# Kernel optimization log

Measured on AMD Instinct MI355X. Metric: run time of the kernel, lower is better.

Reference implementation:

```python
import jax, jax.numpy as jnp
import numpy as np

NUM_EMBEDDINGS = 1024  # num_gestures
EMBEDDING_DIM = 512    # win_size * num_pellets = 32 * 16


def setup_inputs() -> dict:
    key = jax.random.key(0)
    k1, k2 = jax.random.split(key)
    inputs = jax.random.normal(k1, (64, 512, EMBEDDING_DIM), dtype=jnp.float32)
    weight = jax.random.normal(k2, (NUM_EMBEDDINGS, EMBEDDING_DIM), dtype=jnp.float32)
    return {"inputs": inputs, "weight": weight}


def reference(inputs, weight):
    input_shape = inputs.shape
    flat = inputs.reshape(-1, EMBEDDING_DIM)  # [N, D]
    distances = (
        jnp.sum(flat * flat, axis=1, keepdims=True)
        + jnp.sum(weight * weight, axis=1)
        - 2.0 * (flat @ weight.T)
    )
    encoding_indices = jnp.argmin(distances, axis=1)  # [N]
    # one-hot @ weight is just a gather of codebook rows
    quantized = weight[encoding_indices].reshape(input_shape)
    loss_vq = jnp.mean((quantized - inputs) ** 2)
    return loss_vq
```

## Files before the change

### kernel.cpp

```cpp
#include <hip/hip_runtime.h>
#include <hip/hip_bf16.h>
#include <stdint.h>

typedef __attribute__((ext_vector_type(4))) int i32x4;

#define N_ROWS  32768
#define N_CODES 1024
#define DIM     512

typedef const __attribute__((address_space(1))) uint32_t guint;
typedef __attribute__((address_space(3))) uint32_t luint;
static __device__ __forceinline__ void gl_lds16(const char* g, char* l) {
    __builtin_amdgcn_global_load_lds((guint*)g, (luint*)l, 16, 0, 0);
}

static __device__ __forceinline__ int q8(float v) {
    int q = __float2int_rn(v * 32.0f);
    return max(-127, min(127, q));
}

__global__ void __launch_bounds__(256)
convertXW(const float* __restrict__ X, const float* __restrict__ W,
          char* __restrict__ Xq, char* __restrict__ Wq,
          float* __restrict__ xnorm, float* __restrict__ wnorm) {
    const int lane = threadIdx.x & 63;
    const int sub  = threadIdx.x >> 6;
    const float* src; char* dst; float* nrm; int row;
    if (blockIdx.x < 8192) {
        row = blockIdx.x * 4 + sub;
        src = X; dst = Xq; nrm = xnorm;
    } else {
        row = (blockIdx.x - 8192) * 4 + sub;
        src = W; dst = Wq; nrm = wnorm;
    }
    const float4* p = (const float4*)(src + (size_t)row * DIM + lane * 8);
    float4 a = p[0], b = p[1];
    uint32_t lo = (uint32_t)(q8(a.x) & 0xFF)
                | ((uint32_t)(q8(a.y) & 0xFF) << 8)
                | ((uint32_t)(q8(a.z) & 0xFF) << 16)
                | ((uint32_t)(q8(a.w) & 0xFF) << 24);
    uint32_t hi = (uint32_t)(q8(b.x) & 0xFF)
                | ((uint32_t)(q8(b.y) & 0xFF) << 8)
                | ((uint32_t)(q8(b.z) & 0xFF) << 16)
                | ((uint32_t)(q8(b.w) & 0xFF) << 24);
    *(uint2*)(dst + (size_t)row * DIM + lane * 8) = make_uint2(lo, hi);
    float s = a.x*a.x + a.y*a.y + a.z*a.z + a.w*a.w
            + b.x*b.x + b.y*b.y + b.z*b.z + b.w*b.w;
    #pragma unroll
    for (int d = 1; d < 64; d <<= 1) s += __shfl_xor(s, d);
    if (lane == 0) nrm[row] = s;
}

__global__ void __launch_bounds__(256, 2)
gemm_argmin(const char* __restrict__ Xq, const char* __restrict__ Wq,
            const float* __restrict__ wnorm, const float* __restrict__ xnorm,
            float* __restrict__ partial) {
    __shared__ __align__(16) char As[8 * 4096];
    __shared__ __align__(16) char Bs[4 * 3 * 4096];

    const int tid  = threadIdx.x;
    const int lane = tid & 63;
    const int wave = tid >> 6;
    const int lr = lane & 15, kg = lane >> 4;

    const int bid = blockIdx.x;
    const int rowBase = ((bid & 7) * 64 + (bid >> 3)) * 64;
    const int colW = wave * 256;

    const int ssw = ((lane & 3) ^ ((lane >> 3) & 3)) * 16;
    const char* aS = Xq + (size_t)(rowBase + wave * 16 + (lane >> 2)) * DIM + ssw;
    const char* bS = Wq + (size_t)(colW + (lane >> 2)) * DIM + ssw;
    char* bD = Bs + wave * 12288 + lane * 16;

#define STAGE_B(s) do {                                                       \
    const int ctp_ = (s) >> 3, kt_ = (s) & 7, buf_ = (s) % 3;                 \
    _Pragma("unroll")                                                         \
    for (int j = 0; j < 4; ++j)                                               \
        gl_lds16(bS + (size_t)(ctp_ * 64 + j * 16) * DIM + kt_ * 64,          \
                 bD + buf_ * 4096 + j * 1024);                                \
  } while (0)

    #pragma unroll
    for (int kt = 0; kt < 8; ++kt)
        gl_lds16(aS + kt * 64, As + kt * 4096 + wave * 1024 + lane * 16);
    STAGE_B(0);
    STAGE_B(1);
    asm volatile("s_waitcnt vmcnt(4)" ::: "memory");
    __syncthreads();

    i32x4 acc[4][4];
    #pragma unroll
    for (int m = 0; m < 4; ++m)
        #pragma unroll
        for (int n = 0; n < 4; ++n) acc[m][n] = (i32x4)0;
    uint32_t runKey[4][4];
    #pragma unroll
    for (int m = 0; m < 4; ++m)
        #pragma unroll
        for (int r = 0; r < 4; ++r) runKey[m][r] = 0xFFFFFFFFu;

    const int fq = (kg ^ ((lr >> 1) & 3)) * 16;
    const char* bR = Bs + wave * 12288;

    for (int ctp = 0; ctp < 4; ++ctp) {
        #pragma unroll
        for (int kt = 0; kt < 8; ++kt) {
            const int s = ctp * 8 + kt;
            const int buf = s % 3;
            i32x4 aF[4], bF[4];
            #pragma unroll
            for (int m = 0; m < 4; ++m)
                aF[m] = *(const i32x4*)&As[kt * 4096 + (m * 16 + lr) * 64 + fq];
            #pragma unroll
            for (int n = 0; n < 4; ++n)
                bF[n] = *(const i32x4*)&bR[buf * 4096 + (n * 16 + lr) * 64 + fq];
            if (s + 2 < 32) STAGE_B(s + 2);
            #pragma unroll
            for (int m = 0; m < 4; ++m)
                #pragma unroll
                for (int n = 0; n < 4; ++n)
                    acc[m][n] = __builtin_amdgcn_mfma_i32_16x16x64_i8(
                        aF[m], bF[n], acc[m][n], 0, 0, 0);
            if (s + 2 < 32)   asm volatile("s_waitcnt vmcnt(4)" ::: "memory");
            else if (s == 30) asm volatile("s_waitcnt vmcnt(0)" ::: "memory");
        }
        #pragma unroll
        for (int n = 0; n < 4; ++n) {
            const int wcol = colW + ctp * 64 + n * 16 + lr;
            const float wn = wnorm[wcol];
            #pragma unroll
            for (int m = 0; m < 4; ++m)
                #pragma unroll
                for (int r = 0; r < 4; ++r) {
                    float sc = wn - (float)acc[m][n][r] * 0.001953125f;
                    uint32_t u = __float_as_uint(sc);
                    u = (u & 0x80000000u) ? ~u : (u | 0x80000000u);
                    runKey[m][r] = min(runKey[m][r],
                                       (u & ~1023u) | (uint32_t)wcol);
                }
        }
        #pragma unroll
        for (int m = 0; m < 4; ++m)
            #pragma unroll
            for (int n = 0; n < 4; ++n) acc[m][n] = (i32x4)0;
    }
#undef STAGE_B

    uint32_t* kbuf = (uint32_t*)(Bs + wave * 12288);
    #pragma unroll
    for (int m = 0; m < 4; ++m)
        #pragma unroll
        for (int r = 0; r < 4; ++r) {
            uint32_t k = runKey[m][r];
            #pragma unroll
            for (int d = 1; d < 16; d <<= 1)
                k = min(k, (uint32_t)__shfl_xor((int)k, d));
            if (lr == 0) kbuf[m * 16 + kg * 4 + r] = k;
        }
    __syncthreads();

    if (wave == 0) {
        const uint32_t* k0 = (const uint32_t*)(Bs);
        uint32_t k = min(min(k0[lane], k0[3072 + lane]),
                         min(k0[6144 + lane], k0[9216 + lane]));
        uint32_t sb = k & ~1023u;
        float sc = (sb & 0x80000000u) ? __uint_as_float(sb ^ 0x80000000u)
                                      : __uint_as_float(~sb);
        float v = xnorm[rowBase + lane] + sc;
        #pragma unroll
        for (int d = 1; d < 64; d <<= 1) v += __shfl_xor(v, d);
        if (lane == 0) partial[bid] = v;
    }
}

__global__ void __launch_bounds__(256)
finalize(const float* __restrict__ partial, float* __restrict__ out) {
    __shared__ double sm[256];
    sm[threadIdx.x] = (double)partial[threadIdx.x]
                    + (double)partial[threadIdx.x + 256];
    __syncthreads();
    for (int st = 128; st > 0; st >>= 1) {
        if (threadIdx.x < st) sm[threadIdx.x] += sm[threadIdx.x + st];
        __syncthreads();
    }
    if (threadIdx.x == 0)
        out[0] = (float)(sm[0] / (double)((size_t)N_ROWS * DIM));
}

extern "C" void kernel_launch(void* const* d_in, const int* in_sizes, int n_in,
                              void* d_out, int out_size, void* d_ws, size_t ws_size,
                              hipStream_t stream) {
    const float* X = (const float*)d_in[0];
    const float* W = (const float*)d_in[1];
    char* ws = (char*)d_ws;
    char*   Xq      = ws;
    char*   Wq      = ws + 16777216;
    float*  wnorm   = (float*)(ws + 17301504);
    float*  xnorm   = (float*)(ws + 17305600);
    float*  partial = (float*)(ws + 17436672);
    float*  out     = (float*)d_out;

    convertXW<<<8192 + N_CODES / 4, 256, 0, stream>>>(X, W, Xq, Wq, xnorm, wnorm);
    gemm_argmin<<<512, 256, 0, stream>>>(Xq, Wq, wnorm, xnorm, partial);
    finalize<<<1, 256, 0, stream>>>(partial, out);
}
```

Measured before the change: 48.56 us.

## Fuse X quantization and norm computation into the GEMM-argmin kernel

The standalone conversion pass over X is removed. Each GEMM block now loads its 64 fp32 rows directly, computes row norms, quantizes them to int8 and writes them into swizzled LDS. This avoids writing and re-reading the 16MB int8 copy of X plus the xnorm array, and the convert kernel now handles only W. In exchange, the X load in the GEMM prologue is synchronous fp32 register traffic that no longer overlaps with the async B staging as the old global_load_lds path did.

```diff
diff --git a/kernel.cpp b/kernel.cpp
--- a/kernel.cpp
+++ b/kernel.cpp
@@ -18,43 +18,30 @@
     int q = __float2int_rn(v * 32.0f);
     return max(-127, min(127, q));
 }
+static __device__ __forceinline__ uint32_t pack4(float a, float b, float c, float d) {
+    return (uint32_t)(q8(a) & 0xFF) | ((uint32_t)(q8(b) & 0xFF) << 8)
+         | ((uint32_t)(q8(c) & 0xFF) << 16) | ((uint32_t)(q8(d) & 0xFF) << 24);
+}
 
 __global__ void __launch_bounds__(256)
-convertXW(const float* __restrict__ X, const float* __restrict__ W,
-          char* __restrict__ Xq, char* __restrict__ Wq,
-          float* __restrict__ xnorm, float* __restrict__ wnorm) {
+convertW(const float* __restrict__ W, char* __restrict__ Wq,
+         float* __restrict__ wnorm) {
     const int lane = threadIdx.x & 63;
-    const int sub  = threadIdx.x >> 6;
-    const float* src; char* dst; float* nrm; int row;
-    if (blockIdx.x < 8192) {
-        row = blockIdx.x * 4 + sub;
-        src = X; dst = Xq; nrm = xnorm;
-    } else {
-        row = (blockIdx.x - 8192) * 4 + sub;
-        src = W; dst = Wq; nrm = wnorm;
-    }
-    const float4* p = (const float4*)(src + (size_t)row * DIM + lane * 8);
+    const int code = blockIdx.x * 4 + (threadIdx.x >> 6);
+    const float4* p = (const float4*)(W + (size_t)code * DIM + lane * 8);
     float4 a = p[0], b = p[1];
-    uint32_t lo = (uint32_t)(q8(a.x) & 0xFF)
-                | ((uint32_t)(q8(a.y) & 0xFF) << 8)
-                | ((uint32_t)(q8(a.z) & 0xFF) << 16)
-                | ((uint32_t)(q8(a.w) & 0xFF) << 24);
-    uint32_t hi = (uint32_t)(q8(b.x) & 0xFF)
-                | ((uint32_t)(q8(b.y) & 0xFF) << 8)
-                | ((uint32_t)(q8(b.z) & 0xFF) << 16)
-                | ((uint32_t)(q8(b.w) & 0xFF) << 24);
-    *(uint2*)(dst + (size_t)row * DIM + lane * 8) = make_uint2(lo, hi);
+    *(uint2*)(Wq + (size_t)code * DIM + lane * 8) =
+        make_uint2(pack4(a.x, a.y, a.z, a.w), pack4(b.x, b.y, b.z, b.w));
     float s = a.x*a.x + a.y*a.y + a.z*a.z + a.w*a.w
             + b.x*b.x + b.y*b.y + b.z*b.z + b.w*b.w;
     #pragma unroll
     for (int d = 1; d < 64; d <<= 1) s += __shfl_xor(s, d);
-    if (lane == 0) nrm[row] = s;
+    if (lane == 0) wnorm[code] = s;
 }
 
 __global__ void __launch_bounds__(256, 2)
-gemm_argmin(const char* __restrict__ Xq, const char* __restrict__ Wq,
-            const float* __restrict__ wnorm, const float* __restrict__ xnorm,
-            float* __restrict__ partial) {
+gemm_argmin(const float* __restrict__ X, const char* __restrict__ Wq,
+            const float* __restrict__ wnorm, float* __restrict__ partial) {
     __shared__ __align__(16) char As[8 * 4096];
     __shared__ __align__(16) char Bs[4 * 3 * 4096];
 
@@ -68,7 +55,6 @@
     const int colW = wave * 256;
 
     const int ssw = ((lane & 3) ^ ((lane >> 3) & 3)) * 16;
-    const char* aS = Xq + (size_t)(rowBase + wave * 16 + (lane >> 2)) * DIM + ssw;
     const char* bS = Wq + (size_t)(colW + (lane >> 2)) * DIM + ssw;
     char* bD = Bs + wave * 12288 + lane * 16;
 
@@ -80,12 +66,34 @@
                  bD + buf_ * 4096 + j * 1024);                                \
   } while (0)
 
-    #pragma unroll
-    for (int kt = 0; kt < 8; ++kt)
-        gl_lds16(aS + kt * 64, As + kt * 4096 + wave * 1024 + lane * 16);
     STAGE_B(0);
     STAGE_B(1);
-    asm volatile("s_waitcnt vmcnt(4)" ::: "memory");
+
+    const int r = tid >> 2, q4 = tid & 3;
+    const int rsw = (r >> 1) & 3;
+    float nrm = 0.f;
+    {
+        const float* xP = X + (size_t)(rowBase + r) * DIM + q4 * 128;
+        #pragma unroll
+        for (int c = 0; c < 8; ++c) {
+            float4 f0 = *(const float4*)(xP + c * 16);
+            float4 f1 = *(const float4*)(xP + c * 16 + 4);
+            float4 f2 = *(const float4*)(xP + c * 16 + 8);
+            float4 f3 = *(const float4*)(xP + c * 16 + 12);
+            nrm += f0.x*f0.x + f0.y*f0.y + f0.z*f0.z + f0.w*f0.w
+                 + f1.x*f1.x + f1.y*f1.y + f1.z*f1.z + f1.w*f1.w
+                 + f2.x*f2.x + f2.y*f2.y + f2.z*f2.z + f2.w*f2.w
+                 + f3.x*f3.x + f3.y*f3.y + f3.z*f3.z + f3.w*f3.w;
+            i32x4 v = { (int)pack4(f0.x, f0.y, f0.z, f0.w),
+                        (int)pack4(f1.x, f1.y, f1.z, f1.w),
+                        (int)pack4(f2.x, f2.y, f2.z, f2.w),
+                        (int)pack4(f3.x, f3.y, f3.z, f3.w) };
+            const int kt = 2 * q4 + (c >> 2), sl = c & 3;
+            *(i32x4*)&As[kt * 4096 + r * 64 + (sl ^ rsw) * 16] = v;
+        }
+        nrm += __shfl_xor(nrm, 1);
+        nrm += __shfl_xor(nrm, 2);
+    }
     __syncthreads();
 
     i32x4 acc[4][4];
@@ -97,7 +105,7 @@
     #pragma unroll
     for (int m = 0; m < 4; ++m)
         #pragma unroll
-        for (int r = 0; r < 4; ++r) runKey[m][r] = 0xFFFFFFFFu;
+        for (int rr = 0; rr < 4; ++rr) runKey[m][rr] = 0xFFFFFFFFu;
 
     const int fq = (kg ^ ((lr >> 1) & 3)) * 16;
     const char* bR = Bs + wave * 12288;
@@ -131,12 +139,12 @@
             #pragma unroll
             for (int m = 0; m < 4; ++m)
                 #pragma unroll
-                for (int r = 0; r < 4; ++r) {
-                    float sc = wn - (float)acc[m][n][r] * 0.001953125f;
+                for (int rr = 0; rr < 4; ++rr) {
+                    float sc = wn - (float)acc[m][n][rr] * 0.001953125f;
                     uint32_t u = __float_as_uint(sc);
                     u = (u & 0x80000000u) ? ~u : (u | 0x80000000u);
-                    runKey[m][r] = min(runKey[m][r],
-                                       (u & ~1023u) | (uint32_t)wcol);
+                    runKey[m][rr] = min(runKey[m][rr],
+                                        (u & ~1023u) | (uint32_t)wcol);
                 }
         }
         #pragma unroll
@@ -150,13 +158,15 @@
     #pragma unroll
     for (int m = 0; m < 4; ++m)
         #pragma unroll
-        for (int r = 0; r < 4; ++r) {
-            uint32_t k = runKey[m][r];
+        for (int rr = 0; rr < 4; ++rr) {
+            uint32_t k = runKey[m][rr];
             #pragma unroll
             for (int d = 1; d < 16; d <<= 1)
                 k = min(k, (uint32_t)__shfl_xor((int)k, d));
-            if (lr == 0) kbuf[m * 16 + kg * 4 + r] = k;
-        }
+            if (lr == 0) kbuf[m * 16 + kg * 4 + rr] = k;
+        }
+    float* xnS = (float*)(Bs + 48896);
+    if ((tid & 3) == 0) xnS[r] = nrm;
     __syncthreads();
 
     if (wave == 0) {
@@ -166,7 +176,7 @@
         uint32_t sb = k & ~1023u;
         float sc = (sb & 0x80000000u) ? __uint_as_float(sb ^ 0x80000000u)
                                       : __uint_as_float(~sb);
-        float v = xnorm[rowBase + lane] + sc;
+        float v = xnS[lane] + sc;
         #pragma unroll
         for (int d = 1; d < 64; d <<= 1) v += __shfl_xor(v, d);
         if (lane == 0) partial[bid] = v;
@@ -193,14 +203,12 @@
     const float* X = (const float*)d_in[0];
     const float* W = (const float*)d_in[1];
     char* ws = (char*)d_ws;
-    char*   Xq      = ws;
-    char*   Wq      = ws + 16777216;
-    float*  wnorm   = (float*)(ws + 17301504);
-    float*  xnorm   = (float*)(ws + 17305600);
-    float*  partial = (float*)(ws + 17436672);
+    char*   Wq      = ws;
+    float*  wnorm   = (float*)(ws + 524288);
+    float*  partial = (float*)(ws + 528384);
     float*  out     = (float*)d_out;
 
-    convertXW<<<8192 + N_CODES / 4, 256, 0, stream>>>(X, W, Xq, Wq, xnorm, wnorm);
-    gemm_argmin<<<512, 256, 0, stream>>>(Xq, Wq, wnorm, xnorm, partial);
+    convertW<<<N_CODES / 4, 256, 0, stream>>>(W, Wq, wnorm);
+    gemm_argmin<<<512, 256, 0, stream>>>(X, Wq, wnorm, partial);
     finalize<<<1, 256, 0, stream>>>(partial, out);
 }
```

Result: faster. 47.47 us (median of 2 runs) (-2.2%).
